# Kernel optimization log

Hardware: AMD Instinct MI355X
Metric: run time of the kernel (lower is better)

Reference implementation:

```python
import jax, jax.numpy as jnp
import numpy as np

QKV_DIM = 256
C = 32
N_HEAD = 8
OUT_DIM = 256
B1, B2, N = 1, 128, 256


def setup_inputs() -> dict:
    key = jax.random.key(0)
    ks = jax.random.split(key, 8)
    hc = N_HEAD * C
    return {
        "in_data": jax.random.normal(ks[0], (B1, B2, N, QKV_DIM), jnp.float32),
        "mask": jnp.ones((B1, B2, N), jnp.float32),
        "nonbatched_bias": jax.random.normal(ks[1], (B1, N_HEAD, N, N), jnp.float32),
        "w_qkv": jax.random.normal(ks[2], (3 * hc, QKV_DIM), jnp.float32) * (1.0 / np.sqrt(QKV_DIM)),
        "w_gate": jax.random.normal(ks[3], (hc, QKV_DIM), jnp.float32) * 0.02,
        "gating_bias": jnp.ones((hc,), jnp.float32),
        "w_o": jax.random.normal(ks[4], (OUT_DIM, hc), jnp.float32) * 0.02,
        "b_o": jnp.zeros((OUT_DIM,), jnp.float32),
    }


def reference(in_data, mask, nonbatched_bias, w_qkv, w_gate, gating_bias, w_o, b_o):
    scaling = C ** (-0.5)
    # fused QKV projection: [b1,b2,n,3*h*c]
    qkv = jnp.einsum("abnd,ed->abne", in_data, w_qkv)
    q, k, v = jnp.split(qkv, 3, axis=-1)

    def to_heads(t):  # b1 b2 n (h d) -> b1 b2 h n d
        b1, b2, n, _ = t.shape
        return t.reshape(b1, b2, n, N_HEAD, C).transpose(0, 1, 3, 2, 4)

    q, k, v = to_heads(q) * scaling, to_heads(k), to_heads(v)
    # logits: [b1,b2,h,q,k]
    logits = jnp.einsum("abhqd,abhkd->abhqk", q, k)
    mask_bias = (mask[:, :, None, None, :] - 1.0) * 1e9
    logits = logits + mask_bias + nonbatched_bias[:, None]  # broadcast bias over b2
    weights = jax.nn.softmax(logits, axis=-1)
    weighted_avg = jnp.einsum("abhqk,abhkd->abhqd", weights, v)
    b1, b2, h, n, d = weighted_avg.shape
    weighted_avg = weighted_avg.transpose(0, 1, 3, 2, 4).reshape(b1, b2, n, h * d)
    # sigmoid gating
    gate = jax.nn.sigmoid(jnp.einsum("abnd,ed->abne", in_data, w_gate) + gating_bias)
    weighted_avg = gate * weighted_avg
    return jnp.einsum("abne,oe->abno", weighted_avg, w_o) + b_o
```

## Files before the change

### kernel.cpp

```cpp
#include <hip/hip_runtime.h>
#include <hip/hip_bf16.h>
#include <math.h>

#define B2      128
#define NSEQ    256
#define DMODEL  256
#define NHEAD   8
#define CDIM    32
#define HC      256
#define NROWS   (B2*NSEQ)
#define SCALING 0.17677669529663687f

typedef __attribute__((ext_vector_type(8))) short bf16x8;
typedef __attribute__((ext_vector_type(4))) float f32x4;

static __device__ __forceinline__ ushort f2bf(float f) {
    __hip_bfloat16 b = __float2bfloat16(f);
    ushort r; __builtin_memcpy(&r, &b, 2); return r;
}
static __device__ __forceinline__ float bf2f(ushort u) {
    __hip_bfloat16 b; __builtin_memcpy(&b, &u, 2); return __bfloat162float(b);
}
static __device__ __forceinline__ void gload_lds16(const void* g, void* l) {
    __builtin_amdgcn_global_load_lds((const __attribute__((address_space(1))) void*)g,
                                     (__attribute__((address_space(3))) void*)l, 16, 0, 0);
}

__global__ __launch_bounds__(256) void convert_kernel(
    const float* __restrict__ X, const float* __restrict__ Wqkv,
    const float* __restrict__ Wg, const float* __restrict__ Wo,
    ushort* __restrict__ xb, ushort* __restrict__ wqkvgb, ushort* __restrict__ wob)
{
    const int NX = 8388608 / 4, NQ = 196608 / 4, NG = 65536 / 4, NO = 65536 / 4;
    const int total = NX + NQ + NG + NO;
    for (int idx = blockIdx.x * 256 + threadIdx.x; idx < total; idx += gridDim.x * 256) {
        const float* src; ushort* dst; int off; float scale = 1.0f;
        if (idx < NX)                { src = X;    dst = xb;              off = idx; }
        else if (idx < NX + NQ)      { src = Wqkv; dst = wqkvgb;          off = idx - NX;
                                       if (off < 16384) scale = SCALING; }
        else if (idx < NX + NQ + NG) { src = Wg;   dst = wqkvgb + 196608; off = idx - NX - NQ; }
        else                         { src = Wo;   dst = wob;             off = idx - NX - NQ - NG; }
        float4 v = ((const float4*)src)[off];
        union { ushort u[4]; uint2 q; } p;
        p.u[0] = f2bf(v.x * scale); p.u[1] = f2bf(v.y * scale);
        p.u[2] = f2bf(v.z * scale); p.u[3] = f2bf(v.w * scale);
        *(uint2*)(dst + (size_t)off * 4) = p.q;
    }
}

__global__ __launch_bounds__(256) void qkvg_mfma_kernel(
    const ushort* __restrict__ Xb,
    const ushort* __restrict__ Wb,
    const float* __restrict__ gbias,
    ushort* __restrict__ q_ws,
    ushort* __restrict__ k_ws,
    ushort* __restrict__ v_ws,
    ushort* __restrict__ g_ws)
{
    __shared__ ushort S[20480];
    ushort* const Wbuf[2] = { S,        S + 10240 };
    ushort* const Xbuf[2] = { S + 8192, S + 18432 };

    const int tid  = threadIdx.x;
    const int w    = tid >> 6;
    const int lane = tid & 63;
    const int lj   = lane & 15;
    const int lg   = lane >> 4;
    const int m0   = blockIdx.x * 64;
    const int seg  = blockIdx.y;
    const int e0g  = seg * 256;

    f32x4 acc[4][4];
    #pragma unroll
    for (int i = 0; i < 4; ++i)
        #pragma unroll
        for (int j = 0; j < 4; ++j) acc[i][j] = (f32x4){0.f, 0.f, 0.f, 0.f};

    const int srow = lane >> 2;
    const int scol = (((lane & 3) ^ ((lane >> 3) & 3)) << 3);
    const int xsl  = ((lg ^ ((lj >> 1) & 3)) << 3);

    #define QSTAGE(Wdst, Xdst, kk) do {                                          \
        _Pragma("unroll")                                                        \
        for (int c = 0; c < 4; ++c) {                                            \
            const int ci = w * 4 + c;                                            \
            gload_lds16(Wb + (size_t)(e0g + ci * 16 + srow) * 256 + (kk) + scol, \
                        (char*)(Wdst) + ci * 1024);                              \
        }                                                                        \
        gload_lds16(Xb + (size_t)(m0 + w * 16 + srow) * 256 + (kk) + scol,       \
                    (char*)(Xdst) + w * 1024);                                   \
    } while (0)

    QSTAGE(Wbuf[0], Xbuf[0], 0);
    asm volatile("s_waitcnt vmcnt(0)" ::: "memory");
    __builtin_amdgcn_s_barrier();

    #pragma unroll
    for (int t = 0; t < 8; ++t) {
        ushort* Wc = Wbuf[t & 1];
        ushort* Xc = Xbuf[t & 1];
        if (t < 7) QSTAGE(Wbuf[(t + 1) & 1], Xbuf[(t + 1) & 1], (t + 1) * 32);
        bf16x8 af[4], bfr[4];
        #pragma unroll
        for (int i = 0; i < 4; ++i)
            af[i] = *(const bf16x8*)(Wc + (w * 64 + i * 16 + lj) * 32 + xsl);
        #pragma unroll
        for (int j = 0; j < 4; ++j)
            bfr[j] = *(const bf16x8*)(Xc + (j * 16 + lj) * 32 + xsl);
        #pragma unroll
        for (int i = 0; i < 4; ++i)
            #pragma unroll
            for (int j = 0; j < 4; ++j)
                acc[i][j] = __builtin_amdgcn_mfma_f32_16x16x32_bf16(af[i], bfr[j], acc[i][j], 0, 0, 0);
        asm volatile("s_waitcnt vmcnt(0)" ::: "memory");
        __builtin_amdgcn_s_barrier();
    }
    #undef QSTAGE

    uint* T = (uint*)S;
    #pragma unroll
    for (int i = 0; i < 4; ++i) {
        const int el0 = w * 64 + i * 16 + lg * 4;
        #pragma unroll
        for (int j = 0; j < 4; ++j) {
            const int ml = j * 16 + lj;
            union { ushort u[4]; uint2 v; } pk;
            if (seg == 3) {
                #pragma unroll
                for (int r = 0; r < 4; ++r) {
                    const float z = acc[i][j][r] + gbias[el0 + r];
                    pk.u[r] = f2bf(1.f / (1.f + __expf(-z)));
                }
            } else {
                #pragma unroll
                for (int r = 0; r < 4; ++r) pk.u[r] = f2bf(acc[i][j][r]);
            }
            const int wd = (ml * 128 + (el0 >> 1)) ^ ((ml & 7) << 2);
            *(uint2*)(T + wd) = pk.v;
        }
    }
    __syncthreads();

    const int b2 = m0 >> 8;
    const int n0 = m0 & 255;
    if (seg < 3) {
        ushort* base = (seg == 0) ? q_ws : (seg == 1) ? k_ws : v_ws;
        #pragma unroll
        for (int hh = 0; hh < 2; ++hh) {
            const int h = w * 2 + hh;
            ushort* gdst = base + ((size_t)(b2 * 8 + h) * 256 + n0) * 32;
            #pragma unroll
            for (int it = 0; it < 4; ++it) {
                const int ml = it * 16 + (lane >> 2);
                const int cq = lane & 3;
                const int wd = (ml * 128 + h * 16 + cq * 4) ^ ((ml & 7) << 2);
                const uint4 d = *(const uint4*)(T + wd);
                *(uint4*)(gdst + (size_t)ml * 32 + cq * 8) = d;
            }
        }
    } else {
        const int row  = tid >> 2;
        const int part = tid & 3;
        ushort* gdst = g_ws + (size_t)(m0 + row) * 256;
        #pragma unroll
        for (int r8 = 0; r8 < 8; ++r8) {
            const int wc = r8 * 16 + part * 4;
            const int wd = (row * 128 + wc) ^ ((row & 7) << 2);
            const uint4 d = *(const uint4*)(T + wd);
            *(uint4*)(gdst + wc * 2) = d;
        }
    }
}

#define SWZ(c) ((((c) >> 2) & 3) << 5)

__global__ __launch_bounds__(512) void attn_mfma_kernel(
    const ushort* __restrict__ q_ws,
    const ushort* __restrict__ k_ws,
    const ushort* __restrict__ v_ws,
    const ushort* __restrict__ g_ws,
    const float* __restrict__ bias,
    const float* __restrict__ mask,
    ushort* __restrict__ wa_ws)
{
    __shared__ ushort Ks[256 * 32];
    __shared__ ushort Vt[32 * 256];
    __shared__ ushort Pl[8 * 16 * 64];

    const int tid  = threadIdx.x;
    const int bh   = blockIdx.x >> 1;
    const int half = blockIdx.x & 1;
    const int b2   = bh >> 3;
    const int h    = bh & 7;
    const int w    = tid >> 6;
    const int lane = tid & 63;
    const int lj   = lane & 15;
    const int lg   = lane >> 4;

    {
        const char* gk = (const char*)(k_ws + (size_t)bh * 8192);
        gload_lds16(gk + tid * 16,        (char*)Ks + w * 1024);
        gload_lds16(gk + 8192 + tid * 16, (char*)Ks + 8192 + w * 1024);
    }
    {
        const int cq = tid & 3;
        #pragma unroll
        for (int it = 0; it < 2; ++it) {
            const int n = it * 128 + (tid >> 2);
            uint4 v = *(const uint4*)(v_ws + (size_t)bh * 8192 + n * 32 + cq * 8);
            const ushort* pv = (const ushort*)&v;
            #pragma unroll
            for (int e = 0; e < 8; ++e) {
                const int c = cq * 8 + e;
                const int byte = c * 512 + ((2 * n) ^ SWZ(c));
                Vt[byte >> 1] = pv[e];
            }
        }
    }

    const int q0 = half * 128 + w * 16;
    const bf16x8 qf = *(const bf16x8*)(q_ws + (size_t)bh * 8192 + (size_t)(q0 + lj) * 32 + lg * 8);

    f32x4 acc[16];
    const float* bbase = bias + (size_t)h * 256 * 256;
    const float* mrow  = mask + (size_t)b2 * 256;
    #pragma unroll
    for (int t = 0; t < 16; ++t) {
        const int col = t * 16 + lj;
        const float mterm = (mrow[col] - 1.0f) * 1e9f;
        #pragma unroll
        for (int r = 0; r < 4; ++r) {
            const int qrow = q0 + lg * 4 + r;
            acc[t][r] = bbase[(size_t)qrow * 256 + col] + mterm;
        }
    }

    __syncthreads();

    #pragma unroll
    for (int t = 0; t < 16; ++t) {
        const bf16x8 kf = *(const bf16x8*)(Ks + (t * 16 + lj) * 32 + lg * 8);
        acc[t] = __builtin_amdgcn_mfma_f32_16x16x32_bf16(qf, kf, acc[t], 0, 0, 0);
    }

    float inv[4];
    #pragma unroll
    for (int r = 0; r < 4; ++r) {
        float m = acc[0][r];
        #pragma unroll
        for (int t = 1; t < 16; ++t) m = fmaxf(m, acc[t][r]);
        m = fmaxf(m, __shfl_xor(m, 1));
        m = fmaxf(m, __shfl_xor(m, 2));
        m = fmaxf(m, __shfl_xor(m, 4));
        m = fmaxf(m, __shfl_xor(m, 8));
        float s = 0.f;
        #pragma unroll
        for (int t = 0; t < 16; ++t) {
            float e = __expf(acc[t][r] - m);
            acc[t][r] = e;
            s += e;
        }
        s += __shfl_xor(s, 1);
        s += __shfl_xor(s, 2);
        s += __shfl_xor(s, 4);
        s += __shfl_xor(s, 8);
        inv[r] = 1.0f / s;
    }

    ushort* PlW = Pl + w * 1024;
    f32x4 o0 = {0.f, 0.f, 0.f, 0.f};
    f32x4 o1 = {0.f, 0.f, 0.f, 0.f};
    #pragma unroll
    for (int ch = 0; ch < 4; ++ch) {
        #pragma unroll
        for (int tt = 0; tt < 4; ++tt) {
            const int t = ch * 4 + tt;
            #pragma unroll
            for (int r = 0; r < 4; ++r) {
                const int row  = lg * 4 + r;
                const int byte = row * 128 + ((32 * tt + 2 * lj) ^ (lg << 5));
                PlW[byte >> 1] = f2bf(acc[t][r]);
            }
        }
        #pragma unroll
        for (int kk = 0; kk < 2; ++kk) {
            const int abyte = lj * 128 + ((64 * kk + 16 * lg) ^ SWZ(lj));
            const bf16x8 pa = *(const bf16x8*)(PlW + (abyte >> 1));
            const int ks = ch * 2 + kk;
            {
                const int cr = lj;
                const int vbyte = cr * 512 + ((64 * ks + 16 * lg) ^ SWZ(cr));
                const bf16x8 vb = *(const bf16x8*)(Vt + (vbyte >> 1));
                o0 = __builtin_amdgcn_mfma_f32_16x16x32_bf16(pa, vb, o0, 0, 0, 0);
            }
            {
                const int cr = 16 + lj;
                const int vbyte = cr * 512 + ((64 * ks + 16 * lg) ^ SWZ(cr));
                const bf16x8 vb = *(const bf16x8*)(Vt + (vbyte >> 1));
                o1 = __builtin_amdgcn_mfma_f32_16x16x32_bf16(pa, vb, o1, 0, 0, 0);
            }
        }
    }

    #pragma unroll
    for (int r = 0; r < 4; ++r) {
        const int qrow = q0 + lg * 4 + r;
        const size_t rowbase = ((size_t)(b2 * 256 + qrow)) * 256 + h * 32;
        {
            const float gv = bf2f(g_ws[rowbase + lj]);
            wa_ws[rowbase + lj] = f2bf(o0[r] * inv[r] * gv);
        }
        {
            const float gv = bf2f(g_ws[rowbase + 16 + lj]);
            wa_ws[rowbase + 16 + lj] = f2bf(o1[r] * inv[r] * gv);
        }
    }
}

__global__ __launch_bounds__(256) void out_mfma_kernel(
    const ushort* __restrict__ WA,
    const ushort* __restrict__ Wob,
    const float* __restrict__ bo,
    float* __restrict__ out)
{
    __shared__ ushort S[20480];
    ushort* const Obuf[2] = { S,        S + 10240 };
    ushort* const Abuf[2] = { S + 8192, S + 18432 };

    const int tid  = threadIdx.x;
    const int w    = tid >> 6;
    const int lane = tid & 63;
    const int lj   = lane & 15;
    const int lg   = lane >> 4;
    const int m0   = blockIdx.x * 64;

    f32x4 acc[4][4];
    #pragma unroll
    for (int i = 0; i < 4; ++i)
        #pragma unroll
        for (int j = 0; j < 4; ++j) acc[i][j] = (f32x4){0.f, 0.f, 0.f, 0.f};

    const int srow = lane >> 2;
    const int scol = (((lane & 3) ^ ((lane >> 3) & 3)) << 3);
    const int xsl  = ((lg ^ ((lj >> 1) & 3)) << 3);

    #define OSTAGE(Odst, Adst, kk) do {                                          \
        _Pragma("unroll")                                                        \
        for (int c = 0; c < 4; ++c) {                                            \
            const int ci = w * 4 + c;                                            \
            gload_lds16(Wob + (size_t)(ci * 16 + srow) * 256 + (kk) + scol,      \
                        (char*)(Odst) + ci * 1024);                              \
        }                                                                        \
        gload_lds16(WA + (size_t)(m0 + w * 16 + srow) * 256 + (kk) + scol,       \
                    (char*)(Adst) + w * 1024);                                   \
    } while (0)

    OSTAGE(Obuf[0], Abuf[0], 0);
    asm volatile("s_waitcnt vmcnt(0)" ::: "memory");
    __builtin_amdgcn_s_barrier();

    #pragma unroll
    for (int t = 0; t < 8; ++t) {
        ushort* Oc = Obuf[t & 1];
        ushort* Ac = Abuf[t & 1];
        if (t < 7) OSTAGE(Obuf[(t + 1) & 1], Abuf[(t + 1) & 1], (t + 1) * 32);
        bf16x8 af[4], bfr[4];
        #pragma unroll
        for (int i = 0; i < 4; ++i)
            af[i] = *(const bf16x8*)(Ac + (i * 16 + lj) * 32 + xsl);
        #pragma unroll
        for (int j = 0; j < 4; ++j)
            bfr[j] = *(const bf16x8*)(Oc + (w * 64 + j * 16 + lj) * 32 + xsl);
        #pragma unroll
        for (int i = 0; i < 4; ++i)
            #pragma unroll
            for (int j = 0; j < 4; ++j)
                acc[i][j] = __builtin_amdgcn_mfma_f32_16x16x32_bf16(af[i], bfr[j], acc[i][j], 0, 0, 0);
        asm volatile("s_waitcnt vmcnt(0)" ::: "memory");
        __builtin_amdgcn_s_barrier();
    }
    #undef OSTAGE

    #pragma unroll
    for (int i = 0; i < 4; ++i) {
        #pragma unroll
        for (int r = 0; r < 4; ++r) {
            const int m = m0 + i * 16 + lg * 4 + r;
            #pragma unroll
            for (int j = 0; j < 4; ++j) {
                const int o = w * 64 + j * 16 + lj;
                out[(size_t)m * 256 + o] = acc[i][j][r] + bo[o];
            }
        }
    }
}

extern "C" void kernel_launch(void* const* d_in, const int* in_sizes, int n_in,
                              void* d_out, int out_size, void* d_ws, size_t ws_size,
                              hipStream_t stream) {
    const float* in_data = (const float*)d_in[0];
    const float* mask    = (const float*)d_in[1];
    const float* nb_bias = (const float*)d_in[2];
    const float* w_qkv   = (const float*)d_in[3];
    const float* w_gate  = (const float*)d_in[4];
    const float* g_bias  = (const float*)d_in[5];
    const float* w_o     = (const float*)d_in[6];
    const float* b_o     = (const float*)d_in[7];
    float* out = (float*)d_out;

    ushort* ws = (ushort*)d_ws;
    const size_t per_head = (size_t)B2 * NHEAD * NSEQ * CDIM;
    ushort* q_ws   = ws;
    ushort* k_ws   = q_ws + per_head;
    ushort* v_ws   = k_ws + per_head;
    ushort* g_ws   = v_ws + per_head;
    ushort* wa_ws  = g_ws + (size_t)NROWS * HC;
    ushort* xb     = wa_ws + (size_t)NROWS * HC;
    ushort* wqkvgb = xb + (size_t)NROWS * DMODEL;
    ushort* wob    = wqkvgb + 1024 * 256;

    convert_kernel<<<dim3(2048), 256, 0, stream>>>(
        in_data, w_qkv, w_gate, w_o, xb, wqkvgb, wob);

    qkvg_mfma_kernel<<<dim3(NROWS / 64, 4), 256, 0, stream>>>(
        xb, wqkvgb, g_bias, q_ws, k_ws, v_ws, g_ws);

    attn_mfma_kernel<<<dim3(B2 * NHEAD * 2), 512, 0, stream>>>(
        q_ws, k_ws, v_ws, g_ws, nb_bias, mask, wa_ws);

    out_mfma_kernel<<<dim3(NROWS / 64), 256, 0, stream>>>(
        wa_ws, wob, b_o, out);
}
```

Before: 99.40 us.

## Keep X tile resident across QKVG segments and transpose logits in attention

The QKV/gate projection kernel now loads the full 64x256 X tile into LDS once. It then loops over the four weight segments inside one block instead of launching a separate block per segment, removing three redundant X reads from global memory. The cost is a 4x smaller grid and a larger LDS footprint, which may lower occupancy and parallelism. The attention kernel swaps the MFMA operands to compute transposed logits, so bias and mask can be read with float4 loads, the softmax reductions need fewer shuffles, and P is written to LDS with packed 8-byte stores.

```diff
diff --git a/kernel.cpp b/kernel.cpp
--- a/kernel.cpp
+++ b/kernel.cpp
@@ -57,9 +57,9 @@
     ushort* __restrict__ v_ws,
     ushort* __restrict__ g_ws)
 {
-    __shared__ ushort S[20480];
-    ushort* const Wbuf[2] = { S,        S + 10240 };
-    ushort* const Xbuf[2] = { S + 8192, S + 18432 };
+    __shared__ ushort S[32768];
+    ushort* const Wbuf[2] = { S, S + 8192 };
+    ushort* const Xls     = S + 16384;
 
     const int tid  = threadIdx.x;
     const int w    = tid >> 6;
@@ -67,109 +67,114 @@
     const int lj   = lane & 15;
     const int lg   = lane >> 4;
     const int m0   = blockIdx.x * 64;
-    const int seg  = blockIdx.y;
-    const int e0g  = seg * 256;
-
-    f32x4 acc[4][4];
-    #pragma unroll
-    for (int i = 0; i < 4; ++i)
-        #pragma unroll
-        for (int j = 0; j < 4; ++j) acc[i][j] = (f32x4){0.f, 0.f, 0.f, 0.f};
 
     const int srow = lane >> 2;
     const int scol = (((lane & 3) ^ ((lane >> 3) & 3)) << 3);
     const int xsl  = ((lg ^ ((lj >> 1) & 3)) << 3);
 
-    #define QSTAGE(Wdst, Xdst, kk) do {                                          \
+    {
+        const ushort* xsrc = Xb + (size_t)(m0 + (tid >> 2)) * 256 + scol;
+        #pragma unroll
+        for (int t = 0; t < 8; ++t)
+            gload_lds16(xsrc + t * 32, (char*)S + 32768 + t * 4096 + w * 1024);
+    }
+
+    #define WSTAGE(dst, seg, kk) do {                                            \
         _Pragma("unroll")                                                        \
         for (int c = 0; c < 4; ++c) {                                            \
-            const int ci = w * 4 + c;                                            \
-            gload_lds16(Wb + (size_t)(e0g + ci * 16 + srow) * 256 + (kk) + scol, \
-                        (char*)(Wdst) + ci * 1024);                              \
-        }                                                                        \
-        gload_lds16(Xb + (size_t)(m0 + w * 16 + srow) * 256 + (kk) + scol,       \
-                    (char*)(Xdst) + w * 1024);                                   \
-    } while (0)
-
-    QSTAGE(Wbuf[0], Xbuf[0], 0);
-    asm volatile("s_waitcnt vmcnt(0)" ::: "memory");
-    __builtin_amdgcn_s_barrier();
-
-    #pragma unroll
-    for (int t = 0; t < 8; ++t) {
-        ushort* Wc = Wbuf[t & 1];
-        ushort* Xc = Xbuf[t & 1];
-        if (t < 7) QSTAGE(Wbuf[(t + 1) & 1], Xbuf[(t + 1) & 1], (t + 1) * 32);
-        bf16x8 af[4], bfr[4];
+            const int ci = w * 4 + c;       \
+            gload_lds16(Wb + (size_t)((seg) * 256 + ci * 16 + srow) * 256 + (kk) + scol, \
+                        (char*)(dst) + ci * 1024);                               \
+        } } while (0)
+
+    const int b2 = m0 >> 8;
+    const int n0 = m0 & 255;
+
+    for (int seg = 0; seg < 4; ++seg) {
+        f32x4 acc[4][4];
         #pragma unroll
         for (int i = 0; i < 4; ++i)
-            af[i] = *(const bf16x8*)(Wc + (w * 64 + i * 16 + lj) * 32 + xsl);
-        #pragma unroll
-        for (int j = 0; j < 4; ++j)
-            bfr[j] = *(const bf16x8*)(Xc + (j * 16 + lj) * 32 + xsl);
-        #pragma unroll
-        for (int i = 0; i < 4; ++i)
-            #pragma unroll
-            for (int j = 0; j < 4; ++j)
-                acc[i][j] = __builtin_amdgcn_mfma_f32_16x16x32_bf16(af[i], bfr[j], acc[i][j], 0, 0, 0);
+            #pragma unroll
+            for (int j = 0; j < 4; ++j) acc[i][j] = (f32x4){0.f, 0.f, 0.f, 0.f};
+
+        WSTAGE(Wbuf[0], seg, 0);
         asm volatile("s_waitcnt vmcnt(0)" ::: "memory");
         __builtin_amdgcn_s_barrier();
-    }
-    #undef QSTAGE
-
-    uint* T = (uint*)S;
-    #pragma unroll
-    for (int i = 0; i < 4; ++i) {
-        const int el0 = w * 64 + i * 16 + lg * 4;
-        #pragma unroll
-        for (int j = 0; j < 4; ++j) {
-            const int ml = j * 16 + lj;
-            union { ushort u[4]; uint2 v; } pk;
-            if (seg == 3) {
+
+        #pragma unroll
+        for (int t = 0; t < 8; ++t) {
+            ushort* Wc = Wbuf[t & 1];
+            if (t < 7) WSTAGE(Wbuf[(t + 1) & 1], seg, (t + 1) * 32);
+            bf16x8 af[4], bfr[4];
+            #pragma unroll
+            for (int i = 0; i < 4; ++i)
+                af[i] = *(const bf16x8*)(Wc + (w * 64 + i * 16 + lj) * 32 + xsl);
+            #pragma unroll
+            for (int j = 0; j < 4; ++j)
+                bfr[j] = *(const bf16x8*)(Xls + t * 2048 + (j * 16 + lj) * 32 + xsl);
+            #pragma unroll
+            for (int i = 0; i < 4; ++i)
                 #pragma unroll
-                for (int r = 0; r < 4; ++r) {
-                    const float z = acc[i][j][r] + gbias[el0 + r];
-                    pk.u[r] = f2bf(1.f / (1.f + __expf(-z)));
+                for (int j = 0; j < 4; ++j)
+                    acc[i][j] = __builtin_amdgcn_mfma_f32_16x16x32_bf16(af[i], bfr[j], acc[i][j], 0, 0, 0);
+            asm volatile("s_waitcnt vmcnt(0)" ::: "memory");
+            __builtin_amdgcn_s_barrier();
+        }
+
+        uint* T = (uint*)S;
+        #pragma unroll
+        for (int i = 0; i < 4; ++i) {
+            const int el0 = w * 64 + i * 16 + lg * 4;
+            #pragma unroll
+            for (int j = 0; j < 4; ++j) {
+                const int ml = j * 16 + lj;
+                union { ushort u[4]; uint2 v; } pk;
+                if (seg == 3) {
+                    #pragma unroll
+                    for (int r = 0; r < 4; ++r) {
+                        const float z = acc[i][j][r] + gbias[el0 + r];
+                        pk.u[r] = f2bf(1.f / (1.f + __expf(-z)));
+                    }
+                } else {
+                    #pragma unroll
+                    for (int r = 0; r < 4; ++r) pk.u[r] = f2bf(acc[i][j][r]);
                 }
-            } else {
+                const int wd = (ml * 128 + (el0 >> 1)) ^ ((ml & 7) << 2);
+                *(uint2*)(T + wd) = pk.v;
+            }
+        }
+        __syncthreads();
+
+        if (seg < 3) {
+            ushort* base = (seg == 0) ? q_ws : (seg == 1) ? k_ws : v_ws;
+            #pragma unroll
+            for (int hh = 0; hh < 2; ++hh) {
+                const int h = w * 2 + hh;
+                ushort* gdst = base + ((size_t)(b2 * 8 + h) * 256 + n0) * 32;
                 #pragma unroll
-                for (int r = 0; r < 4; ++r) pk.u[r] = f2bf(acc[i][j][r]);
-            }
-            const int wd = (ml * 128 + (el0 >> 1)) ^ ((ml & 7) << 2);
-            *(uint2*)(T + wd) = pk.v;
-        }
-    }
-    __syncthreads();
-
-    const int b2 = m0 >> 8;
-    const int n0 = m0 & 255;
-    if (seg < 3) {
-        ushort* base = (seg == 0) ? q_ws : (seg == 1) ? k_ws : v_ws;
-        #pragma unroll
-        for (int hh = 0; hh < 2; ++hh) {
-            const int h = w * 2 + hh;
-            ushort* gdst = base + ((size_t)(b2 * 8 + h) * 256 + n0) * 32;
-            #pragma unroll
-            for (int it = 0; it < 4; ++it) {
-                const int ml = it * 16 + (lane >> 2);
-                const int cq = lane & 3;
-                const int wd = (ml * 128 + h * 16 + cq * 4) ^ ((ml & 7) << 2);
+                for (int it = 0; it < 4; ++it) {
+                    const int ml = it * 16 + (lane >> 2);
+                    const int cq = lane & 3;
+                    const int wd = (ml * 128 + h * 16 + cq * 4) ^ ((ml & 7) << 2);
+                    const uint4 d = *(const uint4*)(T + wd);
+                    *(uint4*)(gdst + (size_t)ml * 32 + cq * 8) = d;
+                }
+            }
+        } else {
+            const int row  = tid >> 2;
+            const int part = tid & 3;
+            ushort* gdst = g_ws + (size_t)(m0 + row) * 256;
+            #pragma unroll
+            for (int r8 = 0; r8 < 8; ++r8) {
+                const int wc = r8 * 16 + part * 4;
+                const int wd = (row * 128 + wc) ^ ((row & 7) << 2);
                 const uint4 d = *(const uint4*)(T + wd);
-                *(uint4*)(gdst + (size_t)ml * 32 + cq * 8) = d;
-            }
-        }
-    } else {
-        const int row  = tid >> 2;
-        const int part = tid & 3;
-        ushort* gdst = g_ws + (size_t)(m0 + row) * 256;
-        #pragma unroll
-        for (int r8 = 0; r8 < 8; ++r8) {
-            const int wc = r8 * 16 + part * 4;
-            const int wd = (row * 128 + wc) ^ ((row & 7) << 2);
-            const uint4 d = *(const uint4*)(T + wd);
-            *(uint4*)(gdst + wc * 2) = d;
-        }
-    }
+                *(uint4*)(gdst + wc * 2) = d;
+            }
+        }
+        __syncthreads();
+    }
+    #undef WSTAGE
 }
 
 #define SWZ(c) ((((c) >> 2) & 3) << 5)
@@ -185,7 +190,7 @@
 {
     __shared__ ushort Ks[256 * 32];
     __shared__ ushort Vt[32 * 256];
-    __shared__ ushort Pl[8 * 16 * 64];
+    __shared__ ushort Pl[8 * 1024];
 
     const int tid  = threadIdx.x;
     const int bh   = blockIdx.x >> 1;
@@ -222,17 +227,16 @@
     const bf16x8 qf = *(const bf16x8*)(q_ws + (size_t)bh * 8192 + (size_t)(q0 + lj) * 32 + lg * 8);
 
     f32x4 acc[16];
-    const float* bbase = bias + (size_t)h * 256 * 256;
-    const float* mrow  = mask + (size_t)b2 * 256;
+    const float* brow = bias + (size_t)h * 65536 + (size_t)(q0 + lj) * 256;
+    const float* mrow = mask + (size_t)b2 * 256;
     #pragma unroll
     for (int t = 0; t < 16; ++t) {
-        const int col = t * 16 + lj;
-        const float mterm = (mrow[col] - 1.0f) * 1e9f;
-        #pragma unroll
-        for (int r = 0; r < 4; ++r) {
-            const int qrow = q0 + lg * 4 + r;
-            acc[t][r] = bbase[(size_t)qrow * 256 + col] + mterm;
-        }
+        const float4 bv = *(const float4*)(brow + t * 16 + lg * 4);
+        const float4 mv = *(const float4*)(mrow + t * 16 + lg * 4);
+        acc[t][0] = bv.x + (mv.x - 1.0f) * 1e9f;
+        acc[t][1] = bv.y + (mv.y - 1.0f) * 1e9f;
+        acc[t][2] = bv.z + (mv.z - 1.0f) * 1e9f;
+        acc[t][3] = bv.w + (mv.w - 1.0f) * 1e9f;
     }
 
     __syncthreads();
@@ -240,32 +244,31 @@
     #pragma unroll
     for (int t = 0; t < 16; ++t) {
         const bf16x8 kf = *(const bf16x8*)(Ks + (t * 16 + lj) * 32 + lg * 8);
-        acc[t] = __builtin_amdgcn_mfma_f32_16x16x32_bf16(qf, kf, acc[t], 0, 0, 0);
-    }
-
-    float inv[4];
-    #pragma unroll
-    for (int r = 0; r < 4; ++r) {
-        float m = acc[0][r];
-        #pragma unroll
-        for (int t = 1; t < 16; ++t) m = fmaxf(m, acc[t][r]);
-        m = fmaxf(m, __shfl_xor(m, 1));
-        m = fmaxf(m, __shfl_xor(m, 2));
-        m = fmaxf(m, __shfl_xor(m, 4));
-        m = fmaxf(m, __shfl_xor(m, 8));
-        float s = 0.f;
-        #pragma unroll
-        for (int t = 0; t < 16; ++t) {
-            float e = __expf(acc[t][r] - m);
+        acc[t] = __builtin_amdgcn_mfma_f32_16x16x32_bf16(kf, qf, acc[t], 0, 0, 0);
+    }
+
+    float mx = -1e30f;
+    #pragma unroll
+    for (int t = 0; t < 16; ++t)
+        #pragma unroll
+        for (int r = 0; r < 4; ++r) mx = fmaxf(mx, acc[t][r]);
+    mx = fmaxf(mx, __shfl_xor(mx, 16));
+    mx = fmaxf(mx, __shfl_xor(mx, 32));
+    float s = 0.f;
+    #pragma unroll
+    for (int t = 0; t < 16; ++t)
+        #pragma unroll
+        for (int r = 0; r < 4; ++r) {
+            const float e = __expf(acc[t][r] - mx);
             acc[t][r] = e;
             s += e;
         }
-        s += __shfl_xor(s, 1);
-        s += __shfl_xor(s, 2);
-        s += __shfl_xor(s, 4);
-        s += __shfl_xor(s, 8);
-        inv[r] = 1.0f / s;
-    }
+    s += __shfl_xor(s, 16);
+    s += __shfl_xor(s, 32);
+    const float inv = 1.0f / s;
+    float inv_r[4];
+    #pragma unroll
+    for (int r = 0; r < 4; ++r) inv_r[r] = __shfl(inv, lg * 4 + r);
 
     ushort* PlW = Pl + w * 1024;
     f32x4 o0 = {0.f, 0.f, 0.f, 0.f};
@@ -273,18 +276,17 @@
     #pragma unroll
     for (int ch = 0; ch < 4; ++ch) {
         #pragma unroll
-        for (int tt = 0; tt < 4; ++tt) {
-            const int t = ch * 4 + tt;
-            #pragma unroll
-            for (int r = 0; r < 4; ++r) {
-                const int row  = lg * 4 + r;
-                const int byte = row * 128 + ((32 * tt + 2 * lj) ^ (lg << 5));
-                PlW[byte >> 1] = f2bf(acc[t][r]);
-            }
+        for (int tl = 0; tl < 4; ++tl) {
+            const int t = ch * 4 + tl;
+            union { ushort u[4]; uint2 v; } pk;
+            pk.u[0] = f2bf(acc[t][0]); pk.u[1] = f2bf(acc[t][1]);
+            pk.u[2] = f2bf(acc[t][2]); pk.u[3] = f2bf(acc[t][3]);
+            const int byte = (lj * 128 + tl * 32 + lg * 8) ^ ((lj & 7) << 4);
+            *(uint2*)(PlW + (byte >> 1)) = pk.v;
         }
         #pragma unroll
         for (int kk = 0; kk < 2; ++kk) {
-            const int abyte = lj * 128 + ((64 * kk + 16 * lg) ^ SWZ(lj));
+            const int abyte = (lj * 128 + kk * 64 + lg * 16) ^ ((lj & 7) << 4);
             const bf16x8 pa = *(const bf16x8*)(PlW + (abyte >> 1));
             const int ks = ch * 2 + kk;
             {
@@ -308,11 +310,11 @@
         const size_t rowbase = ((size_t)(b2 * 256 + qrow)) * 256 + h * 32;
         {
             const float gv = bf2f(g_ws[rowbase + lj]);
-            wa_ws[rowbase + lj] = f2bf(o0[r] * inv[r] * gv);
+            wa_ws[rowbase + lj] = f2bf(o0[r] * inv_r[r] * gv);
         }
         {
             const float gv = bf2f(g_ws[rowbase + 16 + lj]);
-            wa_ws[rowbase + 16 + lj] = f2bf(o1[r] * inv[r] * gv);
+            wa_ws[rowbase + 16 + lj] = f2bf(o1[r] * inv_r[r] * gv);
         }
     }
 }
@@ -422,7 +424,7 @@
     convert_kernel<<<dim3(2048), 256, 0, stream>>>(
         in_data, w_qkv, w_gate, w_o, xb, wqkvgb, wob);
 
-    qkvg_mfma_kernel<<<dim3(NROWS / 64, 4), 256, 0, stream>>>(
+    qkvg_mfma_kernel<<<dim3(NROWS / 64), 256, 0, stream>>>(
         xb, wqkvgb, g_bias, q_ws, k_ws, v_ws, g_ws);
 
     attn_mfma_kernel<<<dim3(B2 * NHEAD * 2), 512, 0, stream>>>(
```

Result: slower. 108.1 us (+8.8%).

## Fuse X fp32-to-bf16 conversion into QKVG GEMM and widen attention blocks

Applied to the files above, without the earlier changes.

The QKVG projection kernel now reads fp32 input rows directly, converts them to bf16 into a resident LDS tile once, and loops over all four weight segments per block. This removes the separate conversion pass over X, along with its workspace write and re-read, and the 4x redundant X reloads. The convert kernel now handles only the weights. Attention blocks grow to 1024 threads, so one block covers all 256 queries of a head and K/V are staged once per head rather than twice. The trade-offs are a 4x smaller GEMM grid with more serial work per block, higher LDS use, and lower occupancy per block in attention.

```diff
diff --git a/kernel.cpp b/kernel.cpp
--- a/kernel.cpp
+++ b/kernel.cpp
@@ -26,30 +26,27 @@
                                      (__attribute__((address_space(3))) void*)l, 16, 0, 0);
 }
 
-__global__ __launch_bounds__(256) void convert_kernel(
-    const float* __restrict__ X, const float* __restrict__ Wqkv,
-    const float* __restrict__ Wg, const float* __restrict__ Wo,
-    ushort* __restrict__ xb, ushort* __restrict__ wqkvgb, ushort* __restrict__ wob)
+__global__ __launch_bounds__(256) void convertW_kernel(
+    const float* __restrict__ Wqkv, const float* __restrict__ Wg,
+    const float* __restrict__ Wo,
+    ushort* __restrict__ wqkvgb, ushort* __restrict__ wob)
 {
-    const int NX = 8388608 / 4, NQ = 196608 / 4, NG = 65536 / 4, NO = 65536 / 4;
-    const int total = NX + NQ + NG + NO;
-    for (int idx = blockIdx.x * 256 + threadIdx.x; idx < total; idx += gridDim.x * 256) {
-        const float* src; ushort* dst; int off; float scale = 1.0f;
-        if (idx < NX)                { src = X;    dst = xb;              off = idx; }
-        else if (idx < NX + NQ)      { src = Wqkv; dst = wqkvgb;          off = idx - NX;
-                                       if (off < 16384) scale = SCALING; }
-        else if (idx < NX + NQ + NG) { src = Wg;   dst = wqkvgb + 196608; off = idx - NX - NQ; }
-        else                         { src = Wo;   dst = wob;             off = idx - NX - NQ - NG; }
-        float4 v = ((const float4*)src)[off];
-        union { ushort u[4]; uint2 q; } p;
-        p.u[0] = f2bf(v.x * scale); p.u[1] = f2bf(v.y * scale);
-        p.u[2] = f2bf(v.z * scale); p.u[3] = f2bf(v.w * scale);
-        *(uint2*)(dst + (size_t)off * 4) = p.q;
-    }
+    const int NQ = 196608 / 4, NG = 65536 / 4, NO = 65536 / 4;
+    const int idx = blockIdx.x * 256 + threadIdx.x;
+    const float* src; ushort* dst; int off; float scale = 1.0f;
+    if (idx < NQ)           { src = Wqkv; dst = wqkvgb;          off = idx;
+                              if (off < 16384) scale = SCALING; }
+    else if (idx < NQ + NG) { src = Wg;   dst = wqkvgb + 196608; off = idx - NQ; }
+    else                    { src = Wo;   dst = wob;             off = idx - NQ - NG; }
+    float4 v = ((const float4*)src)[off];
+    union { ushort u[4]; uint2 q; } p;
+    p.u[0] = f2bf(v.x * scale); p.u[1] = f2bf(v.y * scale);
+    p.u[2] = f2bf(v.z * scale); p.u[3] = f2bf(v.w * scale);
+    *(uint2*)(dst + (size_t)off * 4) = p.q;
 }
 
 __global__ __launch_bounds__(256) void qkvg_mfma_kernel(
-    const ushort* __restrict__ Xb,
+    const float* __restrict__ X,
     const ushort* __restrict__ Wb,
     const float* __restrict__ gbias,
     ushort* __restrict__ q_ws,
@@ -57,9 +54,9 @@
     ushort* __restrict__ v_ws,
     ushort* __restrict__ g_ws)
 {
-    __shared__ ushort S[20480];
-    ushort* const Wbuf[2] = { S,        S + 10240 };
-    ushort* const Xbuf[2] = { S + 8192, S + 18432 };
+    __shared__ ushort S[32768];
+    ushort* const Wbuf[2] = { S, S + 8192 };
+    ushort* const Xls     = S + 16384;
 
     const int tid  = threadIdx.x;
     const int w    = tid >> 6;
@@ -67,114 +64,130 @@
     const int lj   = lane & 15;
     const int lg   = lane >> 4;
     const int m0   = blockIdx.x * 64;
-    const int seg  = blockIdx.y;
-    const int e0g  = seg * 256;
-
-    f32x4 acc[4][4];
-    #pragma unroll
-    for (int i = 0; i < 4; ++i)
-        #pragma unroll
-        for (int j = 0; j < 4; ++j) acc[i][j] = (f32x4){0.f, 0.f, 0.f, 0.f};
 
     const int srow = lane >> 2;
     const int scol = (((lane & 3) ^ ((lane >> 3) & 3)) << 3);
     const int xsl  = ((lg ^ ((lj >> 1) & 3)) << 3);
 
-    #define QSTAGE(Wdst, Xdst, kk) do {                                          \
+    {
+        const int row  = tid >> 2;
+        const int slot = tid & 3;
+        const int g8   = (slot ^ ((row >> 1) & 3)) * 8;
+        const float* xsrc = X + (size_t)(m0 + row) * 256 + g8;
+        ushort* xdst = Xls + row * 32 + slot * 8;
+        #pragma unroll
+        for (int t = 0; t < 8; ++t) {
+            const float4 a = *(const float4*)(xsrc + t * 32);
+            const float4 b = *(const float4*)(xsrc + t * 32 + 4);
+            union { ushort u[8]; uint4 v; } pk;
+            pk.u[0] = f2bf(a.x); pk.u[1] = f2bf(a.y);
+            pk.u[2] = f2bf(a.z); pk.u[3] = f2bf(a.w);
+            pk.u[4] = f2bf(b.x); pk.u[5] = f2bf(b.y);
+            pk.u[6] = f2bf(b.z); pk.u[7] = f2bf(b.w);
+            *(uint4*)(xdst + t * 2048) = pk.v;
+        }
+    }
+
+    #define WSTAGE(dst, seg, kk) do {                                            \
         _Pragma("unroll")                                                        \
         for (int c = 0; c < 4; ++c) {                                            \
             const int ci = w * 4 + c;                                            \
-            gload_lds16(Wb + (size_t)(e0g + ci * 16 + srow) * 256 + (kk) + scol, \
-                        (char*)(Wdst) + ci * 1024);                              \
-        }                                                                        \
-        gload_lds16(Xb + (size_t)(m0 + w * 16 + srow) * 256 + (kk) + scol,       \
-                    (char*)(Xdst) + w * 1024);                                   \
-    } while (0)
-
-    QSTAGE(Wbuf[0], Xbuf[0], 0);
-    asm volatile("s_waitcnt vmcnt(0)" ::: "memory");
-    __builtin_amdgcn_s_barrier();
-
-    #pragma unroll
-    for (int t = 0; t < 8; ++t) {
-        ushort* Wc = Wbuf[t & 1];
-        ushort* Xc = Xbuf[t & 1];
-        if (t < 7) QSTAGE(Wbuf[(t + 1) & 1], Xbuf[(t + 1) & 1], (t + 1) * 32);
-        bf16x8 af[4], bfr[4];
-        #pragma unroll
-        for (int i = 0; i < 4; ++i)
-            af[i] = *(const bf16x8*)(Wc + (w * 64 + i * 16 + lj) * 32 + xsl);
-        #pragma unroll
-        for (int j = 0; j < 4; ++j)
-            bfr[j] = *(const bf16x8*)(Xc + (j * 16 + lj) * 32 + xsl);
-        #pragma unroll
-        for (int i = 0; i < 4; ++i)
-            #pragma unroll
-            for (int j = 0; j < 4; ++j)
-                acc[i][j] = __builtin_amdgcn_mfma_f32_16x16x32_bf16(af[i], bfr[j], acc[i][j], 0, 0, 0);
-        asm volatile("s_waitcnt vmcnt(0)" ::: "memory");
-        __builtin_amdgcn_s_barrier();
-    }
-    #undef QSTAGE
-
-    uint* T = (uint*)S;
-    #pragma unroll
-    for (int i = 0; i < 4; ++i) {
-        const int el0 = w * 64 + i * 16 + lg * 4;
-        #pragma unroll
-        for (int j = 0; j < 4; ++j) {
-            const int ml = j * 16 + lj;
-            union { ushort u[4]; uint2 v; } pk;
-            if (seg == 3) {
-                #pragma unroll
-                for (int r = 0; r < 4; ++r) {
-                    const float z = acc[i][j][r] + gbias[el0 + r];
-                    pk.u[r] = f2bf(1.f / (1.f + __expf(-z)));
-                }
-            } else {
-                #pragma unroll
-                for (int r = 0; r < 4; ++r) pk.u[r] = f2bf(acc[i][j][r]);
-            }
-            const int wd = (ml * 128 + (el0 >> 1)) ^ ((ml & 7) << 2);
-            *(uint2*)(T + wd) = pk.v;
-        }
-    }
-    __syncthreads();
+            gload_lds16(Wb + (size_t)((seg) * 256 + ci * 16 + srow) * 256 + (kk) + scol, \
+                        (char*)(dst) + ci * 1024);                               \
+        } } while (0)
 
     const int b2 = m0 >> 8;
     const int n0 = m0 & 255;
-    if (seg < 3) {
-        ushort* base = (seg == 0) ? q_ws : (seg == 1) ? k_ws : v_ws;
-        #pragma unroll
-        for (int hh = 0; hh < 2; ++hh) {
-            const int h = w * 2 + hh;
-            ushort* gdst = base + ((size_t)(b2 * 8 + h) * 256 + n0) * 32;
-            #pragma unroll
-            for (int it = 0; it < 4; ++it) {
-                const int ml = it * 16 + (lane >> 2);
-                const int cq = lane & 3;
-                const int wd = (ml * 128 + h * 16 + cq * 4) ^ ((ml & 7) << 2);
+
+    for (int seg = 0; seg < 4; ++seg) {
+        f32x4 acc[4][4];
+        #pragma unroll
+        for (int i = 0; i < 4; ++i)
+            #pragma unroll
+            for (int j = 0; j < 4; ++j) acc[i][j] = (f32x4){0.f, 0.f, 0.f, 0.f};
+
+        WSTAGE(Wbuf[0], seg, 0);
+        __syncthreads();
+
+        #pragma unroll
+        for (int t = 0; t < 8; ++t) {
+            ushort* Wc = Wbuf[t & 1];
+            if (t < 7) WSTAGE(Wbuf[(t + 1) & 1], seg, (t + 1) * 32);
+            bf16x8 af[4], bfr[4];
+            #pragma unroll
+            for (int i = 0; i < 4; ++i)
+                af[i] = *(const bf16x8*)(Wc + (w * 64 + i * 16 + lj) * 32 + xsl);
+            #pragma unroll
+            for (int j = 0; j < 4; ++j)
+                bfr[j] = *(const bf16x8*)(Xls + t * 2048 + (j * 16 + lj) * 32 + xsl);
+            #pragma unroll
+            for (int i = 0; i < 4; ++i)
+                #pragma unroll
+                for (int j = 0; j < 4; ++j)
+                    acc[i][j] = __builtin_amdgcn_mfma_f32_16x16x32_bf16(af[i], bfr[j], acc[i][j], 0, 0, 0);
+            asm volatile("s_waitcnt vmcnt(0)" ::: "memory");
+            __builtin_amdgcn_s_barrier();
+        }
+
+        uint* T = (uint*)S;
+        #pragma unroll
+        for (int i = 0; i < 4; ++i) {
+            const int el0 = w * 64 + i * 16 + lg * 4;
+            #pragma unroll
+            for (int j = 0; j < 4; ++j) {
+                const int ml = j * 16 + lj;
+                union { ushort u[4]; uint2 v; } pk;
+                if (seg == 3) {
+                    #pragma unroll
+                    for (int r = 0; r < 4; ++r) {
+                        const float z = acc[i][j][r] + gbias[el0 + r];
+                        pk.u[r] = f2bf(1.f / (1.f + __expf(-z)));
+                    }
+                } else {
+                    #pragma unroll
+                    for (int r = 0; r < 4; ++r) pk.u[r] = f2bf(acc[i][j][r]);
+                }
+                const int wd = (ml * 128 + (el0 >> 1)) ^ ((ml & 7) << 2);
+                *(uint2*)(T + wd) = pk.v;
+            }
+        }
+        __syncthreads();
+
+        if (seg < 3) {
+            ushort* base = (seg == 0) ? q_ws : (seg == 1) ? k_ws : v_ws;
+            #pragma unroll
+            for (int hh = 0; hh < 2; ++hh) {
+                const int h = w * 2 + hh;
+                ushort* gdst = base + ((size_t)(b2 * 8 + h) * 256 + n0) * 32;
+                #pragma unroll
+                for (int it = 0; it < 4; ++it) {
+                    const int ml = it * 16 + (lane >> 2);
+                    const int cq = lane & 3;
+                    const int wd = (ml * 128 + h * 16 + cq * 4) ^ ((ml & 7) << 2);
+                    const uint4 d = *(const uint4*)(T + wd);
+                    *(uint4*)(gdst + (size_t)ml * 32 + cq * 8) = d;
+                }
+            }
+        } else {
+            const int row  = tid >> 2;
+            const int part = tid & 3;
+            ushort* gdst = g_ws + (size_t)(m0 + row) * 256;
+            #pragma unroll
+            for (int r8 = 0; r8 < 8; ++r8) {
+                const int wc = r8 * 16 + part * 4;
+                const int wd = (row * 128 + wc) ^ ((row & 7) << 2);
                 const uint4 d = *(const uint4*)(T + wd);
-                *(uint4*)(gdst + (size_t)ml * 32 + cq * 8) = d;
-            }
-        }
-    } else {
-        const int row  = tid >> 2;
-        const int part = tid & 3;
-        ushort* gdst = g_ws + (size_t)(m0 + row) * 256;
-        #pragma unroll
-        for (int r8 = 0; r8 < 8; ++r8) {
-            const int wc = r8 * 16 + part * 4;
-            const int wd = (row * 128 + wc) ^ ((row & 7) << 2);
-            const uint4 d = *(const uint4*)(T + wd);
-            *(uint4*)(gdst + wc * 2) = d;
-        }
-    }
+                *(uint4*)(gdst + wc * 2) = d;
+            }
+        }
+        __syncthreads();
+    }
+    #undef WSTAGE
 }
 
 #define SWZ(c) ((((c) >> 2) & 3) << 5)
 
-__global__ __launch_bounds__(512) void attn_mfma_kernel(
+__global__ __launch_bounds__(1024) void attn_mfma_kernel(
     const ushort* __restrict__ q_ws,
     const ushort* __restrict__ k_ws,
     const ushort* __restrict__ v_ws,
@@ -185,11 +198,10 @@
 {
     __shared__ ushort Ks[256 * 32];
     __shared__ ushort Vt[32 * 256];
-    __shared__ ushort Pl[8 * 16 * 64];
+    __shared__ ushort Pl[16 * 1024];
 
     const int tid  = threadIdx.x;
-    const int bh   = blockIdx.x >> 1;
-    const int half = blockIdx.x & 1;
+    const int bh   = blockIdx.x;
     const int b2   = bh >> 3;
     const int h    = bh & 7;
     const int w    = tid >> 6;
@@ -197,32 +209,26 @@
     const int lj   = lane & 15;
     const int lg   = lane >> 4;
 
-    {
-        const char* gk = (const char*)(k_ws + (size_t)bh * 8192);
-        gload_lds16(gk + tid * 16,        (char*)Ks + w * 1024);
-        gload_lds16(gk + 8192 + tid * 16, (char*)Ks + 8192 + w * 1024);
-    }
+    gload_lds16((const char*)(k_ws + (size_t)bh * 8192) + tid * 16,
+                (char*)Ks + w * 1024);
     {
         const int cq = tid & 3;
-        #pragma unroll
-        for (int it = 0; it < 2; ++it) {
-            const int n = it * 128 + (tid >> 2);
-            uint4 v = *(const uint4*)(v_ws + (size_t)bh * 8192 + n * 32 + cq * 8);
-            const ushort* pv = (const ushort*)&v;
-            #pragma unroll
-            for (int e = 0; e < 8; ++e) {
-                const int c = cq * 8 + e;
-                const int byte = c * 512 + ((2 * n) ^ SWZ(c));
-                Vt[byte >> 1] = pv[e];
-            }
-        }
-    }
-
-    const int q0 = half * 128 + w * 16;
+        const int n  = tid >> 2;
+        uint4 v = *(const uint4*)(v_ws + (size_t)bh * 8192 + n * 32 + cq * 8);
+        const ushort* pv = (const ushort*)&v;
+        #pragma unroll
+        for (int e = 0; e < 8; ++e) {
+            const int c = cq * 8 + e;
+            const int byte = c * 512 + ((2 * n) ^ SWZ(c));
+            Vt[byte >> 1] = pv[e];
+        }
+    }
+
+    const int q0 = w * 16;
     const bf16x8 qf = *(const bf16x8*)(q_ws + (size_t)bh * 8192 + (size_t)(q0 + lj) * 32 + lg * 8);
 
     f32x4 acc[16];
-    const float* bbase = bias + (size_t)h * 256 * 256;
+    const float* bbase = bias + (size_t)h * 65536;
     const float* mrow  = mask + (size_t)b2 * 256;
     #pragma unroll
     for (int t = 0; t < 16; ++t) {
@@ -415,17 +421,16 @@
     ushort* v_ws   = k_ws + per_head;
     ushort* g_ws   = v_ws + per_head;
     ushort* wa_ws  = g_ws + (size_t)NROWS * HC;
-    ushort* xb     = wa_ws + (size_t)NROWS * HC;
-    ushort* wqkvgb = xb + (size_t)NROWS * DMODEL;
+    ushort* wqkvgb = wa_ws + (size_t)NROWS * HC;
     ushort* wob    = wqkvgb + 1024 * 256;
 
-    convert_kernel<<<dim3(2048), 256, 0, stream>>>(
-        in_data, w_qkv, w_gate, w_o, xb, wqkvgb, wob);
-
-    qkvg_mfma_kernel<<<dim3(NROWS / 64, 4), 256, 0, stream>>>(
-        xb, wqkvgb, g_bias, q_ws, k_ws, v_ws, g_ws);
-
-    attn_mfma_kernel<<<dim3(B2 * NHEAD * 2), 512, 0, stream>>>(
+    convertW_kernel<<<dim3(320), 256, 0, stream>>>(
+        w_qkv, w_gate, w_o, wqkvgb, wob);
+
+    qkvg_mfma_kernel<<<dim3(NROWS / 64), 256, 0, stream>>>(
+        in_data, wqkvgb, g_bias, q_ws, k_ws, v_ws, g_ws);
+
+    attn_mfma_kernel<<<dim3(B2 * NHEAD), 1024, 0, stream>>>(
         q_ws, k_ws, v_ws, g_ws, nb_bias, mask, wa_ws);
 
     out_mfma_kernel<<<dim3(NROWS / 64), 256, 0, stream>>>(
```

New measurement: 100.6 us. No clear change (+1.2%).
